# Optimization experiments

Measured on AMD Instinct MI355X. Metric: run time of the kernel, lower is better.

Reference implementation:

```python
import jax, jax.numpy as jnp
import numpy as np

N = 15872   # number of predictions (31 * 512)
D = 129     # 128 image features + 1 objectness score
H = 128     # block MLP hidden width
IN = 2 * D + 1  # neighbor feats + main feats + add_info (IoU)
NUM_BLOCKS = 2


def _lin(k, fi, fo):
    return jax.random.normal(k, (fi, fo), jnp.float32) / np.sqrt(fi).astype(np.float32)


def setup_inputs() -> dict:
    key = jax.random.key(0)
    ks = jax.random.split(key, 24)
    # ragged neighborhood structure: mean size 16, exactly E = 16*N edges
    sizes = (np.arange(N) % 31) + 1
    E = int(sizes.sum())  # 253952
    rng = np.random.default_rng(0)
    nbr_idx = rng.integers(0, N, size=E).astype(np.int32)
    self_idx = np.repeat(np.arange(N, dtype=np.int32), sizes)  # sorted segment ids

    inp = {
        "interpolated": jax.random.normal(ks[0], (N, D), jnp.float32),
        "add_info": jax.random.uniform(ks[1], (E, 1), dtype=jnp.float32),
        "neighborhood_sizes": jnp.asarray(sizes, jnp.int32),
        "neighborhoods_indexes": jnp.asarray(nbr_idx),
        "self_indexes": jnp.asarray(self_idx),
    }
    # two (block, output) model pairs
    inp["b0_W1"] = _lin(ks[2], IN, H); inp["b0_b1"] = jnp.zeros((H,), jnp.float32)
    inp["b0_W2"] = _lin(ks[3], H, H);  inp["b0_b2"] = jnp.zeros((H,), jnp.float32)
    inp["b0_Wo"] = _lin(ks[4], H, D); inp["b0_bo"] = jnp.zeros((D,), jnp.float32)
    inp["b1_W1"] = _lin(ks[5], IN, H); inp["b1_b1"] = jnp.zeros((H,), jnp.float32)
    inp["b1_W2"] = _lin(ks[6], H, H);  inp["b1_b2"] = jnp.zeros((H,), jnp.float32)
    inp["b1_Wo"] = _lin(ks[7], H, D); inp["b1_bo"] = jnp.zeros((D,), jnp.float32)
    # final layers: 129 -> 64 -> 1
    inp["f_W1"] = _lin(ks[8], D, 64); inp["f_b1"] = jnp.zeros((64,), jnp.float32)
    inp["f_W2"] = _lin(ks[9], 64, 1); inp["f_b2"] = jnp.zeros((1,), jnp.float32)
    return inp


def _lnms_forward(interpolated, add_info, params, nbr_idx, self_idx):
    # params: list of (W1, b1, W2, b2, Wo, bo) per block, plus (fW1, fb1, fW2, fb2)
    for (W1, b1, W2, b2, Wo, bo) in params[:-1]:
        nbr = interpolated[nbr_idx]    # (E, D) gather of neighbor representations
        main = interpolated[self_idx]  # (E, D) gather of owning prediction
        x = jnp.concatenate([nbr, main, add_info], axis=1)  # (E, 2D+1)
        h = jax.nn.relu(x @ W1 + b1)
        h = jax.nn.relu(h @ W2 + b2)   # (E, H) processed neighborhoods
        # ragged per-neighborhood max pool (segments are contiguous/sorted)
        pooled = jax.ops.segment_max(h, self_idx, num_segments=N,
                                     indices_are_sorted=True)  # (N, H)
        block_output = pooled @ Wo + bo  # (N, D)
        interpolated = interpolated + block_output  # residual scatter-update
    fW1, fb1, fW2, fb2 = params[-1]
    return jax.nn.relu(interpolated @ fW1 + fb1) @ fW2 + fb2  # (N, 1)


def reference(interpolated, add_info,
              b0_W1, b0_b1, b0_W2, b0_b2, b0_Wo, b0_bo,
              b1_W1, b1_b1, b1_W2, b1_b2, b1_Wo, b1_bo,
              f_W1, f_b1, f_W2, f_b2,
              neighborhood_sizes, neighborhoods_indexes, self_indexes):
    params = [
        (b0_W1, b0_b1, b0_W2, b0_b2, b0_Wo, b0_bo),
        (b1_W1, b1_b1, b1_W2, b1_b2, b1_Wo, b1_bo),
        (f_W1, f_b1, f_W2, f_b2),
    ]
    return _lnms_forward(interpolated, add_info, params,
                         neighborhoods_indexes, self_indexes)
```

## Files before the change

### kernel.cpp

```cpp
#include <hip/hip_runtime.h>

#define NSEG 15872
#define DD 129
#define HH 128
#define NTILE (NSEG / 16)

typedef __attribute__((ext_vector_type(8))) short s16x8;
typedef __attribute__((ext_vector_type(4))) short s16x4;
typedef __attribute__((ext_vector_type(4))) float f32x4;
typedef __attribute__((ext_vector_type(16))) float f32x16;
typedef __attribute__((ext_vector_type(4))) unsigned u32x4;

__device__ __forceinline__ unsigned short f2bf(float x) {
  union { float f; unsigned u; } c; c.f = x;
  unsigned r = c.u + 0x7FFFu + ((c.u >> 16) & 1u);
  return (unsigned short)(r >> 16);
}
__device__ __forceinline__ float bf2f(unsigned short v) {
  union { unsigned u; float f; } c; c.u = ((unsigned)v) << 16; return c.f;
}

__device__ __forceinline__ void packB8(short* out, int idx8, const float* W,
                                       int N, int ld, int ncols, int kLimit,
                                       int rowBase) {
  const int n = (idx8 >> 3) % N;
  const int g = idx8 / (8 * N);
  s16x8 o;
#pragma unroll
  for (int i = 0; i < 8; ++i) {
    const int row = g * 8 + i;
    float v = 0.f;
    if (row < kLimit && n < ncols) v = W[(long)(rowBase + row) * ld + n];
    o[i] = (short)f2bf(v);
  }
  *(s16x8*)(out + idx8) = o;
}

__device__ __forceinline__ void packA1T8(short* out, int idx8, const float* W1) {
  const int unit = idx8 >> 3;
  const int lane = unit & 63;
  const int blk = unit >> 6;
  const int Mblk = blk / 10, ks = blk % 10;
  const int m = Mblk * 32 + (lane & 31);
  const int k0 = ks * 16 + ((lane >> 5) << 3);
  s16x8 o;
#pragma unroll
  for (int i = 0; i < 8; ++i) {
    const int k = k0 + i;
    o[i] = (short)((k < DD) ? f2bf(W1[(long)k * HH + m]) : 0);
  }
  *(s16x8*)(out + idx8) = o;
}

__device__ __forceinline__ void packB2T8(short* out, int idx8, const float* W2) {
  const int unit = idx8 >> 3;
  const int lane = unit & 63;
  const int blk = unit >> 6;
  const int ks = blk >> 2, nb = blk & 3;
  const int n = nb * 32 + (lane & 31);
  const int k0 = ks * 16 + ((lane >> 5) << 3);
  s16x8 o;
#pragma unroll
  for (int i = 0; i < 8; ++i)
    o[i] = (short)f2bf(W2[(long)(k0 + i) * HH + n]);
  *(s16x8*)(out + idx8) = o;
}

#define PACK_IDS 161792
#define TAB_IDS (NSEG * 160)
#define PACKV (PACK_IDS / 8)
#define TABV (TAB_IDS / 8)
#define PTBLK ((PACKV + TABV) / 256)
#define HMBLK (NTILE / 4)
__global__ __launch_bounds__(256) void pack_tab_kernel(
    const float* __restrict__ interp, unsigned short* __restrict__ tab,
    const float* __restrict__ W1b0, const float* __restrict__ W1b1,
    const float* __restrict__ W2b0, const float* __restrict__ W2b1,
    const float* __restrict__ Wob0, const float* __restrict__ Wob1,
    const float* __restrict__ fW1, short* __restrict__ PA1,
    short* __restrict__ PB2, short* __restrict__ PWo,
    short* __restrict__ PW1m, short* __restrict__ PfW1,
    const float* __restrict__ b1, float* __restrict__ Hm,
    const int* __restrict__ sizes, int* __restrict__ offs) {
  __shared__ short w1s[20480];
  const int bid = blockIdx.x;
  if (bid == PTBLK + HMBLK) {
    int* sums = (int*)w1s;
    const int t = threadIdx.x;
    const int base = t * (NSEG / 256);
    int s = 0;
#pragma unroll 8
    for (int i = 0; i < NSEG / 256; ++i) s += sizes[base + i];
    sums[t] = s;
    __syncthreads();
    for (int d = 1; d < 256; d <<= 1) {
      int u = (t >= d) ? sums[t - d] : 0;
      __syncthreads();
      sums[t] += u;
      __syncthreads();
    }
    int a = sums[t] - s;
#pragma unroll 8
    for (int i = 0; i < NSEG / 256; ++i) {
      const int sz = sizes[base + i];
      offs[base + i] = a;
      a += sz;
    }
    if (t == 255) offs[NSEG] = a;
    return;
  }
  if (bid >= PTBLK) {
    const int hb = bid - PTBLK;
    for (int u = threadIdx.x; u < 2560; u += 256)
      packB8(w1s, u * 8, W1b0, 128, 128, 128, 129, 129);
    __syncthreads();
    const int lane = threadIdx.x & 63, w = threadIdx.x >> 6;
    const int lk = lane >> 4, n16 = lane & 15;
    const int tile = hb * 4 + w;
    const float* arow = interp + (long)(tile * 16 + n16) * DD;
    s16x8 A[5];
#pragma unroll
    for (int ks = 0; ks < 5; ++ks) {
      s16x8 o;
#pragma unroll
      for (int i = 0; i < 8; ++i) {
        const int k = ks * 32 + lk * 8 + i;
        o[i] = (short)((k < DD) ? f2bf(arow[k]) : 0);
      }
      A[ks] = o;
    }
    f32x4 C[8];
#pragma unroll
    for (int nf = 0; nf < 8; ++nf) C[nf] = (f32x4){0.f, 0.f, 0.f, 0.f};
#pragma unroll
    for (int ks = 0; ks < 5; ++ks)
#pragma unroll
      for (int nf = 0; nf < 8; ++nf) {
        const s16x8 b = *(const s16x8*)(w1s + (((ks * 4 + lk) * 128) + nf * 16 + n16) * 8);
        C[nf] = __builtin_amdgcn_mfma_f32_16x16x32_bf16(A[ks], b, C[nf], 0, 0, 0);
      }
#pragma unroll
    for (int nf = 0; nf < 8; ++nf) {
      const float bv = b1[nf * 16 + n16];
#pragma unroll
      for (int r = 0; r < 4; ++r)
        Hm[(long)(tile * 16 + lk * 4 + r) * HH + nf * 16 + n16] = C[nf][r] + bv;
    }
    return;
  }
  int vid = bid * 256 + threadIdx.x;
  if (vid < PACKV) {
    int idx = vid * 8;
    if (idx < 40960) {
      packA1T8(PA1 + (idx / 20480) * 20480, idx % 20480,
               (idx < 20480) ? W1b0 : W1b1);
      return;
    }
    idx -= 40960;
    if (idx < 32768) {
      packB2T8(PB2 + (idx / 16384) * 16384, idx % 16384,
               (idx < 16384) ? W2b0 : W2b1);
      return;
    }
    idx -= 32768;
    if (idx < 36864) {
      packB8(PWo + (idx / 18432) * 18432, idx % 18432,
             (idx < 18432) ? Wob0 : Wob1, 144, 129, 129, 128, 0);
      return;
    }
    idx -= 36864;
    if (idx < 40960) {
      packB8(PW1m + (idx / 20480) * 20480, idx % 20480,
             (idx < 20480) ? W1b0 : W1b1, 128, 128, 128, 129, 129);
      return;
    }
    idx -= 40960;
    packB8(PfW1, idx, fW1, 64, 64, 64, 129, 0);
    return;
  }
  vid -= PACKV;
  if (vid < TABV) {
    const int n = vid / 20;
    const int g = vid - n * 20;
    s16x8 o = (s16x8){0, 0, 0, 0, 0, 0, 0, 0};
    if (g < 16) {
      const float* src = interp + (long)n * DD + g * 8;
#pragma unroll
      for (int i = 0; i < 8; ++i) o[i] = (short)f2bf(src[i]);
    } else if (g == 16) {
      o[0] = (short)f2bf(interp[(long)n * DD + 128]);
    }
    *(s16x8*)(tab + (long)vid * 8) = o;
  }
}

__device__ __forceinline__ int pairEdge(int row, int oLo, int sLo, int oHi,
                                        int sHi) {
  int e = (row < sLo) ? (oLo + row) : (oHi + row - sLo);
  if (row >= sLo + sHi) e = oHi + sHi - 1;
  return e;
}

struct PairMeta {
  int segLo, segHi, oLo, sLo, oHi, sHi;
};

__device__ __forceinline__ void loadMeta(int p, PairMeta& M,
                                         const int* __restrict__ offs) {
  M.segLo = p;
  M.segHi = NSEG - 1 - p;
  M.oLo = offs[M.segLo]; M.sLo = offs[M.segLo + 1] - M.oLo;
  M.oHi = offs[M.segHi]; M.sHi = offs[M.segHi + 1] - M.oHi;
}

__device__ __forceinline__ void prefetchEdge(
    const PairMeta& M, int c, const int* __restrict__ nbrIdx,
    const float* __restrict__ iou, int n32, int& nbrow, float& io) {
  const int grow = (c << 5) + n32;
  const int e = pairEdge(grow, M.oLo, M.sLo, M.oHi, M.sHi);
  nbrow = nbrIdx[e];
  io = iou[e];
}

__device__ __forceinline__ void prefetchHm(
    const PairMeta& M, const float* __restrict__ Hm, int n32,
    float* hmLo, float* hmHi) {
#pragma unroll
  for (int q = 0; q < 4; ++q) {
    hmLo[q] = Hm[(long)M.segLo * HH + q * 32 + n32];
    hmHi[q] = Hm[(long)M.segHi * HH + q * 32 + n32];
  }
}

__device__ __forceinline__ void gatherX(const unsigned short* __restrict__ tab,
                                        int nbrow, int half, s16x8* X) {
  const unsigned short* ar = tab + (long)nbrow * 160;
#pragma unroll
  for (int ks = 0; ks < 9; ++ks)
    X[ks] = *(const s16x8*)(ar + ks * 16 + half * 8);
}

__device__ __forceinline__ void gemm1Phase(
    const PairMeta& M, int c, const s16x8* X, float io,
    const short* __restrict__ As1, const float* wvT,
    const float* hmLo, const float* hmHi,
    int lane, int half, int n32, s16x8* A2) {
  const int grow = (c << 5) + n32;
  const short oneBf = (short)0x3F80;
  s16x8 bb = (s16x8){0, 0, 0, 0, 0, 0, 0, 0};
  if (half == 0) {
    const bool lo = grow < M.sLo;
    bb[0] = lo ? oneBf : (short)0;
    bb[1] = bb[0];
    bb[2] = lo ? (short)0 : oneBf;
    bb[3] = bb[2];
    bb[4] = (short)f2bf(io);
  }
#pragma unroll
  for (int Mblk = 0; Mblk < 4; ++Mblk) {
    f32x16 C;
#pragma unroll
    for (int i = 0; i < 16; ++i) C[i] = 0.f;
#pragma unroll
    for (int ks = 0; ks < 9; ++ks) {
      const s16x8 a = *(const s16x8*)(As1 + ((Mblk * 10 + ks) * 64 + lane) * 8);
      C = __builtin_amdgcn_mfma_f32_32x32x16_bf16(a, X[ks], C, 0, 0, 0);
    }
    s16x8 ab = (s16x8){0, 0, 0, 0, 0, 0, 0, 0};
    if (half == 0) {
      const unsigned short p0 = f2bf(hmLo[Mblk]);
      ab[0] = (short)p0;
      ab[1] = (short)f2bf(hmLo[Mblk] - bf2f(p0));
      const unsigned short p1 = f2bf(hmHi[Mblk]);
      ab[2] = (short)p1;
      ab[3] = (short)f2bf(hmHi[Mblk] - bf2f(p1));
      ab[4] = (short)f2bf(wvT[Mblk]);
    }
    C = __builtin_amdgcn_mfma_f32_32x32x16_bf16(ab, bb, C, 0, 0, 0);
    unsigned wv[8];
#pragma unroll
    for (int j = 0; j < 8; ++j) {
      const float lo = fmaxf(C[2 * j], 0.f);
      const float hi = fmaxf(C[2 * j + 1], 0.f);
      asm("v_cvt_pk_bf16_f32 %0, %1, %2" : "=v"(wv[j]) : "v"(lo), "v"(hi));
    }
    asm("v_permlane32_swap_b32 %0, %1" : "+v"(wv[0]), "+v"(wv[2]));
    asm("v_permlane32_swap_b32 %0, %1" : "+v"(wv[1]), "+v"(wv[3]));
    asm("v_permlane32_swap_b32 %0, %1" : "+v"(wv[4]), "+v"(wv[6]));
    asm("v_permlane32_swap_b32 %0, %1" : "+v"(wv[5]), "+v"(wv[7]));
    union { u32x4 u; s16x8 s; } q0, q1;
    q0.u = (u32x4){wv[0], wv[1], wv[2], wv[3]};
    q1.u = (u32x4){wv[4], wv[5], wv[6], wv[7]};
    A2[2 * Mblk] = q0.s;
    A2[2 * Mblk + 1] = q1.s;
  }
}

__device__ __forceinline__ void gemm2Phase(
    const PairMeta& M, int c, const s16x8* A2, const short* __restrict__ Bs2,
    int lane, int half, int n32, float* mxLo, float* mxHi) {
#pragma unroll
  for (int nb = 0; nb < 4; ++nb) {
    f32x16 D;
#pragma unroll
    for (int i = 0; i < 16; ++i) D[i] = 0.f;
#pragma unroll
    for (int ks = 0; ks < 8; ++ks) {
      const s16x8 b = *(const s16x8*)(Bs2 + ((ks * 4 + nb) * 64 + lane) * 8);
      D = __builtin_amdgcn_mfma_f32_32x32x16_bf16(A2[ks], b, D, 0, 0, 0);
    }
#pragma unroll
    for (int reg = 0; reg < 16; ++reg) {
      const int rrow = (reg & 3) + 8 * (reg >> 2) + 4 * half;
      const int gr = (c << 5) + rrow;
      const float v = D[reg];
      if (gr < M.sLo) mxLo[nb] = fmaxf(mxLo[nb], v);
      else            mxHi[nb] = fmaxf(mxHi[nb], v);
    }
  }
}

__global__ __launch_bounds__(512, 2) void edge_kernel(
    const unsigned short* __restrict__ tab, const short* __restrict__ PA1,
    const short* __restrict__ PB2, const float* __restrict__ W1,
    const float* __restrict__ Hm, const float* __restrict__ iou,
    const int* __restrict__ nbrIdx, const int* __restrict__ offs,
    const float* __restrict__ b2, unsigned short* __restrict__ pooled) {
  extern __shared__ __align__(16) char smem[];
  short* As1 = (short*)smem;
  short* Bs2 = (short*)(smem + 40960);
  {
    const f32x4* s1 = (const f32x4*)PA1;
    f32x4* d1 = (f32x4*)As1;
    for (int i = threadIdx.x; i < 2560; i += 512) d1[i] = s1[i];
    const f32x4* s2 = (const f32x4*)PB2;
    f32x4* d2 = (f32x4*)Bs2;
    for (int i = threadIdx.x; i < 2048; i += 512) d2[i] = s2[i];
  }
  __syncthreads();

  const int lane = threadIdx.x & 63;
  const int w = __builtin_amdgcn_readfirstlane(threadIdx.x >> 6);
  const int half = lane >> 5, n32 = lane & 31;

  float b2v[4], wvT[4];
#pragma unroll
  for (int q = 0; q < 4; ++q) {
    b2v[q] = b2[q * 32 + n32];
    wvT[q] = W1[258 * HH + q * 32 + n32];
  }

  const int wid = (blockIdx.x << 3) + w;
  const int nw = gridDim.x << 3;
  const int npairs = NSEG >> 1;

  if (wid >= npairs) return;

  PairMeta M, Mn;
  float io, ioq;
  float hmLo[4], hmHi[4], hmLoN[4], hmHiN[4];
  s16x8 X[9];
  loadMeta(wid, M, offs);
  {
    int nbq;
    prefetchEdge(M, 0, nbrIdx, iou, n32, nbq, io);
    gatherX(tab, nbq, half, X);
  }
  prefetchHm(M, Hm, n32, hmLo, hmHi);

  int p = wid;
  for (;;) {
    s16x8 A2[8];
    gemm1Phase(M, 0, X, io, As1, wvT, hmLo, hmHi, lane, half, n32, A2);
    const int pn = p + nw;
    const bool hn = pn < npairs;
    const bool small = (M.sLo + M.sHi) <= 32;
    if (small && hn) {
      loadMeta(pn, Mn, offs);
      int nbq;
      prefetchEdge(Mn, 0, nbrIdx, iou, n32, nbq, ioq);
      prefetchHm(Mn, Hm, n32, hmLoN, hmHiN);
      gatherX(tab, nbq, half, X);
    }
    float mxLo[4], mxHi[4];
#pragma unroll
    for (int q = 0; q < 4; ++q) { mxLo[q] = -3.4e38f; mxHi[q] = -3.4e38f; }
    gemm2Phase(M, 0, A2, Bs2, lane, half, n32, mxLo, mxHi);
    if (!small) {
      const int nchunk = (M.sLo + M.sHi + 31) >> 5;
      for (int c = 1; c < nchunk; ++c) {
        int nbf; float iof;
        prefetchEdge(M, c, nbrIdx, iou, n32, nbf, iof);
        gatherX(tab, nbf, half, X);
        gemm1Phase(M, c, X, iof, As1, wvT, hmLo, hmHi, lane, half, n32, A2);
        gemm2Phase(M, c, A2, Bs2, lane, half, n32, mxLo, mxHi);
      }
      if (hn) {
        loadMeta(pn, Mn, offs);
        int nbq;
        prefetchEdge(Mn, 0, nbrIdx, iou, n32, nbq, ioq);
        prefetchHm(Mn, Hm, n32, hmLoN, hmHiN);
        gatherX(tab, nbq, half, X);
      }
    }
#pragma unroll
    for (int nb = 0; nb < 4; ++nb) {
      float lo = fmaxf(mxLo[nb], __shfl_xor(mxLo[nb], 32, 64));
      float hi = fmaxf(mxHi[nb], __shfl_xor(mxHi[nb], 32, 64));
      if (half == 0) {
        pooled[(long)M.segLo * HH + nb * 32 + n32] = f2bf(fmaxf(lo + b2v[nb], 0.f));
        pooled[(long)M.segHi * HH + nb * 32 + n32] = f2bf(fmaxf(hi + b2v[nb], 0.f));
      }
    }
    if (!hn) break;
    M = Mn; io = ioq;
#pragma unroll
    for (int q = 0; q < 4; ++q) { hmLo[q] = hmLoN[q]; hmHi[q] = hmHiN[q]; }
    p = pn;
  }
}

template <int NEXT>
__global__ __launch_bounds__(256) void resout_kernel(
    const unsigned short* __restrict__ pooled, const short* __restrict__ PWo,
    const float* __restrict__ bo, const float* __restrict__ resIn,
    float* __restrict__ resOut, unsigned short* __restrict__ tab,
    const short* __restrict__ PW1mN, const float* __restrict__ b1n,
    float* __restrict__ HmOut,
    const short* __restrict__ PfW1, const float* __restrict__ fb1,
    const float* __restrict__ fW2, const float* __restrict__ fb2,
    float* __restrict__ outFinal) {
  __shared__ short stS[4][16 * 168];
  const int lane = threadIdx.x & 63, w = threadIdx.x >> 6;
  const int lk = lane >> 4, n16 = lane & 15;
  short* st = stS[w];

  {
    const int row = lane >> 2, c0 = 129 + (lane & 3) * 8;
#pragma unroll
    for (int i = 0; i < 8; ++i) st[row * 168 + c0 + i] = 0;
  }

  const int tile = blockIdx.x * 4 + w;
  const unsigned short* arow = pooled + (long)(tile * 16 + n16) * HH;
  s16x8 A[4];
#pragma unroll
  for (int ks = 0; ks < 4; ++ks) A[ks] = *(const s16x8*)(arow + ks * 32 + lk * 8);
  f32x4 C[9];
#pragma unroll
  for (int nf = 0; nf < 9; ++nf) C[nf] = (f32x4){0.f, 0.f, 0.f, 0.f};
#pragma unroll
  for (int ks = 0; ks < 4; ++ks)
#pragma unroll
    for (int nf = 0; nf < 9; ++nf) {
      const s16x8 b = *(const s16x8*)(PWo + (((ks * 4 + lk) * 144) + nf * 16 + n16) * 8);
      C[nf] = __builtin_amdgcn_mfma_f32_16x16x32_bf16(A[ks], b, C[nf], 0, 0, 0);
    }

#pragma unroll
  for (int nf = 0; nf < 8; ++nf) {
    const int col = nf * 16 + n16;
    const float bov = bo[col];
#pragma unroll
    for (int r = 0; r < 4; ++r) {
      const int row = lk * 4 + r;
      const long node = tile * 16 + row;
      const float res = resIn[node * DD + col] + bov + C[nf][r];
      if (NEXT) {
        resOut[node * DD + col] = res;
        tab[node * 160 + col] = f2bf(res);
      }
      st[row * 168 + col] = (short)f2bf(res);
    }
  }
  if (n16 == 0) {
#pragma unroll
    for (int r = 0; r < 4; ++r) {
      const int row = lk * 4 + r;
      const long node = tile * 16 + row;
      const float res = resIn[node * DD + 128] + bo[128] + C[8][r];
      if (NEXT) {
        resOut[node * DD + 128] = res;
        tab[node * 160 + 128] = f2bf(res);
      }
      st[row * 168 + 128] = (short)f2bf(res);
    }
  }

  s16x8 A5[5];
#pragma unroll
  for (int ks = 0; ks < 5; ++ks)
    A5[ks] = *(const s16x8*)(st + n16 * 168 + ks * 32 + lk * 8);

  if (NEXT) {
    f32x4 H[8];
#pragma unroll
    for (int nf = 0; nf < 8; ++nf) H[nf] = (f32x4){0.f, 0.f, 0.f, 0.f};
#pragma unroll
    for (int ks = 0; ks < 5; ++ks)
#pragma unroll
      for (int nf = 0; nf < 8; ++nf) {
        const s16x8 b = *(const s16x8*)(PW1mN + (((ks * 4 + lk) * 128) + nf * 16 + n16) * 8);
        H[nf] = __builtin_amdgcn_mfma_f32_16x16x32_bf16(A5[ks], b, H[nf], 0, 0, 0);
      }
#pragma unroll
    for (int nf = 0; nf < 8; ++nf) {
      const float bv = b1n[nf * 16 + n16];
#pragma unroll
      for (int r = 0; r < 4; ++r)
        HmOut[(long)(tile * 16 + lk * 4 + r) * HH + nf * 16 + n16] = H[nf][r] + bv;
    }
  } else {
    f32x4 Ch[4];
#pragma unroll
    for (int nf = 0; nf < 4; ++nf) Ch[nf] = (f32x4){0.f, 0.f, 0.f, 0.f};
#pragma unroll
    for (int ks = 0; ks < 5; ++ks)
#pragma unroll
      for (int nf = 0; nf < 4; ++nf) {
        const s16x8 b = *(const s16x8*)(PfW1 + (((ks * 4 + lk) * 64) + nf * 16 + n16) * 8);
        Ch[nf] = __builtin_amdgcn_mfma_f32_16x16x32_bf16(A5[ks], b, Ch[nf], 0, 0, 0);
      }
    float b1v[4], w2v[4];
#pragma unroll
    for (int nf = 0; nf < 4; ++nf) {
      b1v[nf] = fb1[nf * 16 + n16];
      w2v[nf] = fW2[nf * 16 + n16];
    }
#pragma unroll
    for (int r = 0; r < 4; ++r) {
      float s = 0.f;
#pragma unroll
      for (int nf = 0; nf < 4; ++nf)
        s += fmaxf(Ch[nf][r] + b1v[nf], 0.f) * w2v[nf];
      s += __shfl_xor(s, 1, 64);
      s += __shfl_xor(s, 2, 64);
      s += __shfl_xor(s, 4, 64);
      s += __shfl_xor(s, 8, 64);
      if (n16 == 0) outFinal[tile * 16 + lk * 4 + r] = s + fb2[0];
    }
  }
}

extern "C" void kernel_launch(void* const* d_in, const int* in_sizes, int n_in,
                              void* d_out, int out_size, void* d_ws, size_t ws_size,
                              hipStream_t stream) {
  const float* interp  = (const float*)d_in[0];
  const float* addInfo = (const float*)d_in[1];
  const int* sizes     = (const int*)d_in[2];
  const int* nbrIdx    = (const int*)d_in[3];
  const float* b0W1 = (const float*)d_in[5];
  const float* b0b1 = (const float*)d_in[6];
  const float* b0W2 = (const float*)d_in[7];
  const float* b0b2 = (const float*)d_in[8];
  const float* b0Wo = (const float*)d_in[9];
  const float* b0bo = (const float*)d_in[10];
  const float* b1W1 = (const float*)d_in[11];
  const float* b1b1 = (const float*)d_in[12];
  const float* b1W2 = (const float*)d_in[13];
  const float* b1b2 = (const float*)d_in[14];
  const float* b1Wo = (const float*)d_in[15];
  const float* b1bo = (const float*)d_in[16];
  const float* fW1  = (const float*)d_in[17];
  const float* fb1  = (const float*)d_in[18];
  const float* fW2  = (const float*)d_in[19];
  const float* fb2  = (const float*)d_in[20];

  char* ws = (char*)d_ws;
  int*            offs  = (int*)(ws + 0);
  short*          PA1   = (short*)(ws + 65536);
  short*          PB2   = (short*)(ws + 147456);
  short*          PWo   = (short*)(ws + 212992);
  short*          PW1m  = (short*)(ws + 286720);
  short*          PfW1  = (short*)(ws + 368640);
  unsigned short* TAB   = (unsigned short*)(ws + 393216);
  float*          HM    = (float*)(ws + 5472256);
  unsigned short* POOLED= (unsigned short*)(ws + 13598720);
  float*          RES   = (float*)(ws + 17661952);

  pack_tab_kernel<<<PTBLK + HMBLK + 1, 256, 0, stream>>>(
      interp, TAB, b0W1, b1W1, b0W2, b1W2, b0Wo, b1Wo, fW1,
      PA1, PB2, PWo, PW1m, PfW1, b0b1, HM, sizes, offs);

  const size_t e_lds = 40960 + 32768;

  edge_kernel<<<248, 512, e_lds, stream>>>(TAB, PA1, PB2, b0W1, HM, addInfo,
                                           nbrIdx, offs, b0b2, POOLED);
  resout_kernel<1><<<NTILE / 4, 256, 0, stream>>>(
      POOLED, PWo, b0bo, interp, RES, TAB, PW1m + 20480, b1b1, HM,
      nullptr, nullptr, nullptr, nullptr, nullptr);

  edge_kernel<<<248, 512, e_lds, stream>>>(TAB, PA1 + 20480, PB2 + 16384, b1W1,
                                           HM, addInfo, nbrIdx, offs,
                                           b1b2, POOLED);
  resout_kernel<0><<<NTILE / 4, 256, 0, stream>>>(
      POOLED, PWo + 18432, b1bo, RES, nullptr, nullptr, nullptr, nullptr,
      nullptr, PfW1, fb1, fW2, fb2, (float*)d_out);
}
```

Before: 180.3 us.

## Process two segment pairs per wave with interleaved MFMA chains

Each wave now handles two neighborhood pairs at once, interleaving their independent MFMA accumulation chains so that one chain's latency hides the other's and each LDS weight fragment is reused across both. The gather of neighbor rows moves to the top of each iteration, so only indices, IoU values and Hm are prefetched for the next batch instead of the full X tile. This raises register pressure (two X and A2 sets) under the 512-thread, 2-block launch bound, which risks spills or lower occupancy. Large pairs are still processed serially for their extra chunks.

```diff
diff --git a/kernel.cpp b/kernel.cpp
--- a/kernel.cpp
+++ b/kernel.cpp
@@ -240,6 +240,54 @@
     X[ks] = *(const s16x8*)(ar + ks * 16 + half * 8);
 }
 
+__device__ __forceinline__ void transposeC(const f32x16& C, s16x8* A2out) {
+  unsigned wv[8];
+#pragma unroll
+  for (int j = 0; j < 8; ++j) {
+    const float lo = fmaxf(C[2 * j], 0.f);
+    const float hi = fmaxf(C[2 * j + 1], 0.f);
+    asm("v_cvt_pk_bf16_f32 %0, %1, %2" : "=v"(wv[j]) : "v"(lo), "v"(hi));
+  }
+  asm("v_permlane32_swap_b32 %0, %1" : "+v"(wv[0]), "+v"(wv[2]));
+  asm("v_permlane32_swap_b32 %0, %1" : "+v"(wv[1]), "+v"(wv[3]));
+  asm("v_permlane32_swap_b32 %0, %1" : "+v"(wv[4]), "+v"(wv[6]));
+  asm("v_permlane32_swap_b32 %0, %1" : "+v"(wv[5]), "+v"(wv[7]));
+  union { u32x4 u; s16x8 s; } q0, q1;
+  q0.u = (u32x4){wv[0], wv[1], wv[2], wv[3]};
+  q1.u = (u32x4){wv[4], wv[5], wv[6], wv[7]};
+  A2out[0] = q0.s;
+  A2out[1] = q1.s;
+}
+
+__device__ __forceinline__ void makeBB(const PairMeta& M, float io, int half,
+                                       int n32, s16x8& bb) {
+  const short oneBf = (short)0x3F80;
+  bb = (s16x8){0, 0, 0, 0, 0, 0, 0, 0};
+  if (half == 0) {
+    const bool lo = n32 < M.sLo;
+    bb[0] = lo ? oneBf : (short)0;
+    bb[1] = bb[0];
+    bb[2] = lo ? (short)0 : oneBf;
+    bb[3] = bb[2];
+    bb[4] = (short)f2bf(io);
+  }
+}
+
+__device__ __forceinline__ void makeAB(const float* hmLo, const float* hmHi,
+                                       const float* wvT, int Mblk, int half,
+                                       s16x8& ab) {
+  ab = (s16x8){0, 0, 0, 0, 0, 0, 0, 0};
+  if (half == 0) {
+    const unsigned short p0 = f2bf(hmLo[Mblk]);
+    ab[0] = (short)p0;
+    ab[1] = (short)f2bf(hmLo[Mblk] - bf2f(p0));
+    const unsigned short p1 = f2bf(hmHi[Mblk]);
+    ab[2] = (short)p1;
+    ab[3] = (short)f2bf(hmHi[Mblk] - bf2f(p1));
+    ab[4] = (short)f2bf(wvT[Mblk]);
+  }
+}
+
 __device__ __forceinline__ void gemm1Phase(
     const PairMeta& M, int c, const s16x8* X, float io,
     const short* __restrict__ As1, const float* wvT,
@@ -266,33 +314,10 @@
       const s16x8 a = *(const s16x8*)(As1 + ((Mblk * 10 + ks) * 64 + lane) * 8);
       C = __builtin_amdgcn_mfma_f32_32x32x16_bf16(a, X[ks], C, 0, 0, 0);
     }
-    s16x8 ab = (s16x8){0, 0, 0, 0, 0, 0, 0, 0};
-    if (half == 0) {
-      const unsigned short p0 = f2bf(hmLo[Mblk]);
-      ab[0] = (short)p0;
-      ab[1] = (short)f2bf(hmLo[Mblk] - bf2f(p0));
-      const unsigned short p1 = f2bf(hmHi[Mblk]);
-      ab[2] = (short)p1;
-      ab[3] = (short)f2bf(hmHi[Mblk] - bf2f(p1));
-      ab[4] = (short)f2bf(wvT[Mblk]);
-    }
+    s16x8 ab;
+    makeAB(hmLo, hmHi, wvT, Mblk, half, ab);
     C = __builtin_amdgcn_mfma_f32_32x32x16_bf16(ab, bb, C, 0, 0, 0);
-    unsigned wv[8];
-#pragma unroll
-    for (int j = 0; j < 8; ++j) {
-      const float lo = fmaxf(C[2 * j], 0.f);
-      const float hi = fmaxf(C[2 * j + 1], 0.f);
-      asm("v_cvt_pk_bf16_f32 %0, %1, %2" : "=v"(wv[j]) : "v"(lo), "v"(hi));
-    }
-    asm("v_permlane32_swap_b32 %0, %1" : "+v"(wv[0]), "+v"(wv[2]));
-    asm("v_permlane32_swap_b32 %0, %1" : "+v"(wv[1]), "+v"(wv[3]));
-    asm("v_permlane32_swap_b32 %0, %1" : "+v"(wv[4]), "+v"(wv[6]));
-    asm("v_permlane32_swap_b32 %0, %1" : "+v"(wv[5]), "+v"(wv[7]));
-    union { u32x4 u; s16x8 s; } q0, q1;
-    q0.u = (u32x4){wv[0], wv[1], wv[2], wv[3]};
-    q1.u = (u32x4){wv[4], wv[5], wv[6], wv[7]};
-    A2[2 * Mblk] = q0.s;
-    A2[2 * Mblk + 1] = q1.s;
+    transposeC(C, A2 + 2 * Mblk);
   }
 }
 
@@ -316,6 +341,65 @@
       const float v = D[reg];
       if (gr < M.sLo) mxLo[nb] = fmaxf(mxLo[nb], v);
       else            mxHi[nb] = fmaxf(mxHi[nb], v);
+    }
+  }
+}
+
+__device__ __forceinline__ void gemm1Batch(
+    const PairMeta& MA, const PairMeta& MB,
+    const s16x8* XA, const s16x8* XB, float ioA, float ioB,
+    const short* __restrict__ As1, const float* wvT,
+    const float* hmLoA, const float* hmHiA,
+    const float* hmLoB, const float* hmHiB,
+    int lane, int half, int n32, s16x8* A2A, s16x8* A2B) {
+  s16x8 bbA, bbB;
+  makeBB(MA, ioA, half, n32, bbA);
+  makeBB(MB, ioB, half, n32, bbB);
+#pragma unroll
+  for (int Mblk = 0; Mblk < 4; ++Mblk) {
+    f32x16 CA, CB;
+#pragma unroll
+    for (int i = 0; i < 16; ++i) { CA[i] = 0.f; CB[i] = 0.f; }
+#pragma unroll
+    for (int ks = 0; ks < 9; ++ks) {
+      const s16x8 a = *(const s16x8*)(As1 + ((Mblk * 10 + ks) * 64 + lane) * 8);
+      CA = __builtin_amdgcn_mfma_f32_32x32x16_bf16(a, XA[ks], CA, 0, 0, 0);
+      CB = __builtin_amdgcn_mfma_f32_32x32x16_bf16(a, XB[ks], CB, 0, 0, 0);
+    }
+    s16x8 abA, abB;
+    makeAB(hmLoA, hmHiA, wvT, Mblk, half, abA);
+    makeAB(hmLoB, hmHiB, wvT, Mblk, half, abB);
+    CA = __builtin_amdgcn_mfma_f32_32x32x16_bf16(abA, bbA, CA, 0, 0, 0);
+    CB = __builtin_amdgcn_mfma_f32_32x32x16_bf16(abB, bbB, CB, 0, 0, 0);
+    transposeC(CA, A2A + 2 * Mblk);
+    transposeC(CB, A2B + 2 * Mblk);
+  }
+}
+
+__device__ __forceinline__ void gemm2Batch(
+    const PairMeta& MA, const PairMeta& MB,
+    const s16x8* A2A, const s16x8* A2B, const short* __restrict__ Bs2,
+    int lane, int half, float* mxLoA, float* mxHiA,
+    float* mxLoB, float* mxHiB) {
+#pragma unroll
+  for (int nb = 0; nb < 4; ++nb) {
+    f32x16 DA, DB;
+#pragma unroll
+    for (int i = 0; i < 16; ++i) { DA[i] = 0.f; DB[i] = 0.f; }
+#pragma unroll
+    for (int ks = 0; ks < 8; ++ks) {
+      const s16x8 b = *(const s16x8*)(Bs2 + ((ks * 4 + nb) * 64 + lane) * 8);
+      DA = __builtin_amdgcn_mfma_f32_32x32x16_bf16(A2A[ks], b, DA, 0, 0, 0);
+      DB = __builtin_amdgcn_mfma_f32_32x32x16_bf16(A2B[ks], b, DB, 0, 0, 0);
+    }
+#pragma unroll
+    for (int reg = 0; reg < 16; ++reg) {
+      const int rrow = (reg & 3) + 8 * (reg >> 2) + 4 * half;
+      const float vA = DA[reg], vB = DB[reg];
+      if (rrow < MA.sLo) mxLoA[nb] = fmaxf(mxLoA[nb], vA);
+      else               mxHiA[nb] = fmaxf(mxHiA[nb], vA);
+      if (rrow < MB.sLo) mxLoB[nb] = fmaxf(mxLoB[nb], vB);
+      else               mxHiB[nb] = fmaxf(mxHiB[nb], vB);
     }
   }
 }
@@ -356,66 +440,102 @@
 
   if (wid >= npairs) return;
 
-  PairMeta M, Mn;
-  float io, ioq;
-  float hmLo[4], hmHi[4], hmLoN[4], hmHiN[4];
-  s16x8 X[9];
-  loadMeta(wid, M, offs);
-  {
-    int nbq;
-    prefetchEdge(M, 0, nbrIdx, iou, n32, nbq, io);
-    gatherX(tab, nbq, half, X);
-  }
-  prefetchHm(M, Hm, n32, hmLo, hmHi);
+  PairMeta MA, MB, MA2, MB2;
+  int nbA, nbB;
+  float ioA, ioB;
+  float hmLoA[4], hmHiA[4], hmLoB[4], hmHiB[4];
+  bool curB, nxtB;
+
+  loadMeta(wid, MA, offs);
+  curB = (wid + nw) < npairs;
+  loadMeta(curB ? wid + nw : wid, MB, offs);
+  prefetchEdge(MA, 0, nbrIdx, iou, n32, nbA, ioA);
+  prefetchEdge(MB, 0, nbrIdx, iou, n32, nbB, ioB);
+  prefetchHm(MA, Hm, n32, hmLoA, hmHiA);
+  prefetchHm(MB, Hm, n32, hmLoB, hmHiB);
 
   int p = wid;
   for (;;) {
-    s16x8 A2[8];
-    gemm1Phase(M, 0, X, io, As1, wvT, hmLo, hmHi, lane, half, n32, A2);
-    const int pn = p + nw;
+    s16x8 XA[9], XB[9];
+    gatherX(tab, nbA, half, XA);
+    gatherX(tab, nbB, half, XB);
+    s16x8 A2A[8], A2B[8];
+    gemm1Batch(MA, MB, XA, XB, ioA, ioB, As1, wvT,
+               hmLoA, hmHiA, hmLoB, hmHiB, lane, half, n32, A2A, A2B);
+    const int pn = p + 2 * nw;
     const bool hn = pn < npairs;
-    const bool small = (M.sLo + M.sHi) <= 32;
+    const bool small = (MA.sLo + MA.sHi <= 32) && (MB.sLo + MB.sHi <= 32);
+    nxtB = curB;
     if (small && hn) {
-      loadMeta(pn, Mn, offs);
-      int nbq;
-      prefetchEdge(Mn, 0, nbrIdx, iou, n32, nbq, ioq);
-      prefetchHm(Mn, Hm, n32, hmLoN, hmHiN);
-      gatherX(tab, nbq, half, X);
-    }
-    float mxLo[4], mxHi[4];
-#pragma unroll
-    for (int q = 0; q < 4; ++q) { mxLo[q] = -3.4e38f; mxHi[q] = -3.4e38f; }
-    gemm2Phase(M, 0, A2, Bs2, lane, half, n32, mxLo, mxHi);
+      loadMeta(pn, MA2, offs);
+      nxtB = (pn + nw) < npairs;
+      loadMeta(nxtB ? pn + nw : pn, MB2, offs);
+      prefetchEdge(MA2, 0, nbrIdx, iou, n32, nbA, ioA);
+      prefetchEdge(MB2, 0, nbrIdx, iou, n32, nbB, ioB);
+      prefetchHm(MA2, Hm, n32, hmLoA, hmHiA);
+      prefetchHm(MB2, Hm, n32, hmLoB, hmHiB);
+    }
+    float mxLoA[4], mxHiA[4], mxLoB[4], mxHiB[4];
+#pragma unroll
+    for (int q = 0; q < 4; ++q) {
+      mxLoA[q] = -3.4e38f; mxHiA[q] = -3.4e38f;
+      mxLoB[q] = -3.4e38f; mxHiB[q] = -3.4e38f;
+    }
+    gemm2Batch(MA, MB, A2A, A2B, Bs2, lane, half,
+               mxLoA, mxHiA, mxLoB, mxHiB);
     if (!small) {
-      const int nchunk = (M.sLo + M.sHi + 31) >> 5;
-      for (int c = 1; c < nchunk; ++c) {
-        int nbf; float iof;
-        prefetchEdge(M, c, nbrIdx, iou, n32, nbf, iof);
-        gatherX(tab, nbf, half, X);
-        gemm1Phase(M, c, X, iof, As1, wvT, hmLo, hmHi, lane, half, n32, A2);
-        gemm2Phase(M, c, A2, Bs2, lane, half, n32, mxLo, mxHi);
+      if (MA.sLo + MA.sHi > 32) {
+        const int nchunk = (MA.sLo + MA.sHi + 31) >> 5;
+        for (int c = 1; c < nchunk; ++c) {
+          int nbf; float iof;
+          prefetchEdge(MA, c, nbrIdx, iou, n32, nbf, iof);
+          gatherX(tab, nbf, half, XA);
+          gemm1Phase(MA, c, XA, iof, As1, wvT, hmLoA, hmHiA, lane, half, n32, A2A);
+          gemm2Phase(MA, c, A2A, Bs2, lane, half, n32, mxLoA, mxHiA);
+        }
+      }
+      if (curB && MB.sLo + MB.sHi > 32) {
+        const int nchunk = (MB.sLo + MB.sHi + 31) >> 5;
+        for (int c = 1; c < nchunk; ++c) {
+          int nbf; float iof;
+          prefetchEdge(MB, c, nbrIdx, iou, n32, nbf, iof);
+          gatherX(tab, nbf, half, XB);
+          gemm1Phase(MB, c, XB, iof, As1, wvT, hmLoB, hmHiB, lane, half, n32, A2B);
+          gemm2Phase(MB, c, A2B, Bs2, lane, half, n32, mxLoB, mxHiB);
+        }
       }
       if (hn) {
-        loadMeta(pn, Mn, offs);
-        int nbq;
-        prefetchEdge(Mn, 0, nbrIdx, iou, n32, nbq, ioq);
-        prefetchHm(Mn, Hm, n32, hmLoN, hmHiN);
-        gatherX(tab, nbq, half, X);
+        loadMeta(pn, MA2, offs);
+        nxtB = (pn + nw) < npairs;
+        loadMeta(nxtB ? pn + nw : pn, MB2, offs);
+        prefetchEdge(MA2, 0, nbrIdx, iou, n32, nbA, ioA);
+        prefetchEdge(MB2, 0, nbrIdx, iou, n32, nbB, ioB);
+        prefetchHm(MA2, Hm, n32, hmLoA, hmHiA);
+        prefetchHm(MB2, Hm, n32, hmLoB, hmHiB);
       }
     }
 #pragma unroll
     for (int nb = 0; nb < 4; ++nb) {
-      float lo = fmaxf(mxLo[nb], __shfl_xor(mxLo[nb], 32, 64));
-      float hi = fmaxf(mxHi[nb], __shfl_xor(mxHi[nb], 32, 64));
+      float lo = fmaxf(mxLoA[nb], __shfl_xor(mxLoA[nb], 32, 64));
+      float hi = fmaxf(mxHiA[nb], __shfl_xor(mxHiA[nb], 32, 64));
       if (half == 0) {
-        pooled[(long)M.segLo * HH + nb * 32 + n32] = f2bf(fmaxf(lo + b2v[nb], 0.f));
-        pooled[(long)M.segHi * HH + nb * 32 + n32] = f2bf(fmaxf(hi + b2v[nb], 0.f));
+        pooled[(long)MA.segLo * HH + nb * 32 + n32] = f2bf(fmaxf(lo + b2v[nb], 0.f));
+        pooled[(long)MA.segHi * HH + nb * 32 + n32] = f2bf(fmaxf(hi + b2v[nb], 0.f));
+      }
+    }
+    if (curB) {
+#pragma unroll
+      for (int nb = 0; nb < 4; ++nb) {
+        float lo = fmaxf(mxLoB[nb], __shfl_xor(mxLoB[nb], 32, 64));
+        float hi = fmaxf(mxHiB[nb], __shfl_xor(mxHiB[nb], 32, 64));
+        if (half == 0) {
+          pooled[(long)MB.segLo * HH + nb * 32 + n32] = f2bf(fmaxf(lo + b2v[nb], 0.f));
+          pooled[(long)MB.segHi * HH + nb * 32 + n32] = f2bf(fmaxf(hi + b2v[nb], 0.f));
+        }
       }
     }
     if (!hn) break;
-    M = Mn; io = ioq;
-#pragma unroll
-    for (int q = 0; q < 4; ++q) { hmLo[q] = hmLoN[q]; hmHi[q] = hmHiN[q]; }
+    MA = MA2; MB = MB2; curB = nxtB;
     p = pn;
   }
 }
```

New measurement: 179.8 us. No clear change (-0.3%).
